# Kernel optimization log

Measured on AMD Instinct MI355X. Metric: run time of the kernel, lower is better.

The kernel has to match this reference:

```python
import jax, jax.numpy as jnp
import numpy as np


def _gcn(x, src, dst, W, b, M):
    # GCNConv: out = D^{-1/2} (A+I) D^{-1/2} X W + b, messages flow src->dst
    xw = x @ W  # [M, D]
    loops = jnp.arange(M)
    s = jnp.concatenate([src, loops])
    d = jnp.concatenate([dst, loops])
    deg = jax.ops.segment_sum(jnp.ones_like(s, x.dtype), d, num_segments=M)
    dinv = jnp.where(deg > 0, jax.lax.rsqrt(jnp.maximum(deg, 1.0)), 0.0)
    norm = dinv[s] * dinv[d]  # [Eg+M]
    return jax.ops.segment_sum(norm[:, None] * xw[s], d, num_segments=M) + b


def _graph_cross_attention(values, k, q, e_src, e_dst, N):
    # gather-dot, segment softmax over destination tokens, scatter-sum of values
    scale = jnp.sqrt(jnp.asarray(k.shape[1], k.dtype))
    dots = (q[e_dst] * k[e_src]).sum(-1) / scale  # [Ea]
    m = jax.ops.segment_max(dots, e_dst, num_segments=N)
    m = jnp.where(jnp.isfinite(m), m, 0.0)
    w = jnp.exp(dots - m[e_dst])
    den = jax.ops.segment_sum(w, e_dst, num_segments=N)
    w = w / jnp.where(den > 0, den, 1.0)[e_dst]
    return jax.ops.segment_sum(w[:, None] * values[e_src], e_dst, num_segments=N)


def reference(token_embeddings, tokens2edges, edge_index, e2t_src, e2t_dst,
              W_gnn, b_gnn, Wk, bk, Wq, bq, Wl, bl, gate_a, gate_b):
    N = token_embeddings.shape[1]
    M = tokens2edges.shape[1]

    def per_sample(t, t2e, ei, es, ed):
        edge_emb = t[t2e]                                  # [M, D] gather
        edge_emb = _gcn(edge_emb, ei[0], ei[1], W_gnn, b_gnn, M)
        k = edge_emb @ Wk + bk                             # [M, 64]
        q = t @ Wq + bq                                    # [N, 64]
        gatt = _graph_cross_attention(edge_emb, k, q, es, ed, N)  # [N, D]
        new = t + jnp.tanh(gate_a) * gatt
        new = new + jnp.tanh(gate_b) * (new @ Wl + bl)
        return new

    return jax.vmap(per_sample)(token_embeddings, tokens2edges, edge_index, e2t_src, e2t_dst)


def setup_inputs() -> dict:
    B, N, M, Eg, Ea, D, DK = 4, 4096, 16384, 65536, 65536, 512, 64
    key = jax.random.key(0)
    ks = jax.random.split(key, 16)
    s = 0.05  # weight scale to keep activations well-conditioned
    return {
        "token_embeddings": jax.random.normal(ks[0], (B, N, D), jnp.float32),
        "tokens2edges": jax.random.randint(ks[1], (B, M), 0, N),
        "edge_index": jax.random.randint(ks[2], (B, 2, Eg), 0, M),
        "e2t_src": jax.random.randint(ks[3], (B, Ea), 0, M),
        "e2t_dst": jax.random.randint(ks[4], (B, Ea), 0, N),
        "W_gnn": jax.random.normal(ks[5], (D, D), jnp.float32) * s,
        "b_gnn": jax.random.normal(ks[6], (D,), jnp.float32) * s,
        "Wk": jax.random.normal(ks[7], (D, DK), jnp.float32) * s,
        "bk": jax.random.normal(ks[8], (DK,), jnp.float32) * s,
        "Wq": jax.random.normal(ks[9], (D, DK), jnp.float32) * s,
        "bq": jax.random.normal(ks[10], (DK,), jnp.float32) * s,
        "Wl": jax.random.normal(ks[11], (D, D), jnp.float32) * s,
        "bl": jax.random.normal(ks[12], (D,), jnp.float32) * s,
        "gate_a": jax.random.normal(ks[13], (1,), jnp.float32),
        "gate_b": jax.random.normal(ks[14], (1,), jnp.float32),
    }
```

## Files before the change

### kernel.cpp

```cpp
#include <hip/hip_runtime.h>
#include <math.h>

#define BB 4
#define NT 4096
#define ME 16384
#define EG 65536
#define EA 65536
#define DD 512
#define DKK 64

using bf16x8 = __attribute__((ext_vector_type(8))) short;
using f32x4  = __attribute__((ext_vector_type(4))) float;

static __device__ __forceinline__ unsigned short f2bf(float f) {
    unsigned u = __float_as_uint(f);
    u += 0x7fffu + ((u >> 16) & 1u);
    return (unsigned short)(u >> 16);
}
static __device__ __forceinline__ float bf2f(unsigned short u) {
    return __uint_as_float((unsigned)u << 16);
}
static __device__ __forceinline__ void acc8(float* a, uint4 v, float s) {
    a[0] += s * __uint_as_float(v.x << 16);
    a[1] += s * __uint_as_float(v.x & 0xffff0000u);
    a[2] += s * __uint_as_float(v.y << 16);
    a[3] += s * __uint_as_float(v.y & 0xffff0000u);
    a[4] += s * __uint_as_float(v.z << 16);
    a[5] += s * __uint_as_float(v.z & 0xffff0000u);
    a[6] += s * __uint_as_float(v.w << 16);
    a[7] += s * __uint_as_float(v.w & 0xffff0000u);
}
static __device__ __forceinline__ uint4 pack8(const float* a) {
    uint4 o;
    o.x = (unsigned)f2bf(a[0]) | ((unsigned)f2bf(a[1]) << 16);
    o.y = (unsigned)f2bf(a[2]) | ((unsigned)f2bf(a[3]) << 16);
    o.z = (unsigned)f2bf(a[4]) | ((unsigned)f2bf(a[5]) << 16);
    o.w = (unsigned)f2bf(a[6]) | ((unsigned)f2bf(a[7]) << 16);
    return o;
}

__global__ void k_hist2(const int* __restrict__ ei_all, const int* __restrict__ ed_all,
                        int* __restrict__ cntG, int* __restrict__ cntA) {
    int i = blockIdx.x * 256 + threadIdx.x;
    if (i < BB * EG) {
        int b = i >> 16, e = i & (EG - 1);
        int dst = ei_all[(size_t)b * 2 * EG + EG + e];
        atomicAdd(&cntG[b * ME + dst], 1);
    } else {
        int j = i - BB * EG;
        atomicAdd(&cntA[(j >> 16) * NT + ed_all[j]], 1);
    }
}

__global__ __launch_bounds__(1024) void k_scan2(
    const int* __restrict__ cntG, int* __restrict__ offsG, int* __restrict__ curG,
    float* __restrict__ dinv,
    const int* __restrict__ cntA, int* __restrict__ offsA, int* __restrict__ curA) {
    __shared__ int sums[1024];
    int tid = threadIdx.x;
    int bid = blockIdx.x;
    const int* cnt;
    int *offs, *cur;
    float* dv = nullptr;
    int C, nk;
    if (bid < BB) {
        cnt = cntG + bid * ME; offs = offsG + bid * (ME + 1); cur = curG + bid * ME;
        dv = dinv + bid * ME; C = ME / 1024; nk = ME;
    } else {
        int b = bid - BB;
        cnt = cntA + b * NT; offs = offsA + b * (NT + 1); cur = curA + b * NT;
        C = NT / 1024; nk = NT;
    }
    int local[16];
    int tot = 0;
    for (int i = 0; i < C; ++i) { local[i] = cnt[tid * C + i]; tot += local[i]; }
    sums[tid] = tot;
    __syncthreads();
    for (int d = 1; d < 1024; d <<= 1) {
        int v = (tid >= d) ? sums[tid - d] : 0;
        __syncthreads();
        sums[tid] += v;
        __syncthreads();
    }
    int run = sums[tid] - tot;
    for (int i = 0; i < C; ++i) {
        int idx = tid * C + i;
        offs[idx] = run;
        cur[idx] = run;
        if (dv) dv[idx] = rsqrtf((float)local[i] + 1.0f);
        run += local[i];
    }
    if (tid == 1023) offs[nk] = run;
}

__global__ void k_fill2(const int* __restrict__ ei_all, const int* __restrict__ es_all,
                        const int* __restrict__ ed_all, const int* __restrict__ t2e_all,
                        const float* __restrict__ dinv,
                        int* __restrict__ curG, int2* __restrict__ csrG,
                        int* __restrict__ curA, int2* __restrict__ csrA) {
    int i = blockIdx.x * 256 + threadIdx.x;
    if (i < BB * EG) {
        int b = i >> 16, e = i & (EG - 1);
        const int* ei = ei_all + (size_t)b * 2 * EG;
        int s = ei[e], d = ei[EG + e];
        int p = atomicAdd(&curG[b * ME + d], 1);
        int2 v;
        v.x = t2e_all[(b << 14) + s];
        v.y = __float_as_int(dinv[b * ME + s]);
        csrG[(size_t)b * EG + p] = v;
    } else {
        int j = i - BB * EG;
        int b = j >> 16;
        int p = atomicAdd(&curA[b * NT + ed_all[j]], 1);
        int2 v;
        v.x = es_all[j];
        v.y = ed_all[j];
        csrA[(size_t)b * EA + p] = v;
    }
}

__global__ void k_cast(const float* __restrict__ x, unsigned short* __restrict__ xb) {
    long i = (long)blockIdx.x * blockDim.x + threadIdx.x;
    float4 v = *(const float4*)(x + (i << 2));
    ushort4 o;
    o.x = f2bf(v.x); o.y = f2bf(v.y); o.z = f2bf(v.z); o.w = f2bf(v.w);
    *(ushort4*)(xb + (i << 2)) = o;
}

__global__ void k_wt(const float* __restrict__ W, unsigned short* __restrict__ Wt) {
    int i = blockIdx.x * 256 + threadIdx.x;
    int n = i >> 9, k = i & 511;
    Wt[i] = f2bf(W[((long)k << 9) + n]);
}
__global__ void k_wtT(const float* __restrict__ Wgnn, const float* __restrict__ Wgk,
                      const float* __restrict__ Wq, unsigned short* __restrict__ BtT) {
    int i = blockIdx.x * 256 + threadIdx.x;
    int n = i >> 9, k = i & 511;
    float v;
    if (n < 512)      v = Wgnn[((long)k << 9) + n];
    else if (n < 576) v = Wgk[k * 64 + (n - 512)];
    else              v = Wq[k * 64 + (n - 576)];
    BtT[i] = f2bf(v);
}
__global__ void k_bias(const float* __restrict__ bgnn, const float* __restrict__ Wk,
                       const float* __restrict__ bk, const float* __restrict__ bq,
                       float* __restrict__ biasG, float* __restrict__ bias640) {
    int tid = threadIdx.x;
    if (tid < 512) { biasG[tid] = bgnn[tid]; bias640[tid] = 0.0f; return; }
    if (tid < 576) {
        int n = tid - 512;
        float s = bk[n];
        for (int k = 0; k < DD; ++k) s += bgnn[k] * Wk[k * 64 + n];
        biasG[tid] = s;
        bias640[tid] = 0.0f;
        return;
    }
    bias640[tid] = bq[tid - 576];
}

__global__ __launch_bounds__(256, 2) void gemm_token(
    const unsigned short* __restrict__ A, const unsigned short* __restrict__ BtT,
    const float* __restrict__ bias640, unsigned short* __restrict__ Xg,
    unsigned short* __restrict__ Xk, unsigned short* __restrict__ qmatb)
{
    __shared__ short As[64 * 32];
    __shared__ short Bs[320 * 32];
    int tid = threadIdx.x;
    int lane = tid & 63;
    int w = tid >> 6;
    long bm = (long)blockIdx.x * 64;
    int bcol = blockIdx.y * 320;
    const unsigned short* Bblk = BtT + (long)bcol * DD;

    f32x4 acc[4][5] = {};

    for (int k0 = 0; k0 < DD; k0 += 32) {
        {
            int s = tid;
            int r = s >> 2;
            int gc = ((s & 3) ^ ((s >> 3) & 3)) * 8;
            __builtin_amdgcn_global_load_lds(
                (const __attribute__((address_space(1))) unsigned int*)(A + (bm + r) * DD + k0 + gc),
                (__attribute__((address_space(3))) unsigned int*)(As + s * 8), 16, 0, 0);
        }
#pragma unroll
        for (int i = 0; i < 5; ++i) {
            int s = tid + i * 256;
            int r = s >> 2;
            int gc = ((s & 3) ^ ((s >> 3) & 3)) * 8;
            __builtin_amdgcn_global_load_lds(
                (const __attribute__((address_space(1))) unsigned int*)(Bblk + (long)r * DD + k0 + gc),
                (__attribute__((address_space(3))) unsigned int*)(Bs + s * 8), 16, 0, 0);
        }
        __syncthreads();

        int cq = lane >> 4;
        bf16x8 af[4];
#pragma unroll
        for (int rb = 0; rb < 4; ++rb) {
            int r = rb * 16 + (lane & 15);
            af[rb] = *(const bf16x8*)&As[(r * 4 + (cq ^ ((r >> 1) & 3))) * 8];
        }
#pragma unroll
        for (int cb = 0; cb < 5; ++cb) {
            int r = w * 80 + cb * 16 + (lane & 15);
            bf16x8 bf = *(const bf16x8*)&Bs[(r * 4 + (cq ^ ((r >> 1) & 3))) * 8];
#pragma unroll
            for (int rb = 0; rb < 4; ++rb)
                acc[rb][cb] = __builtin_amdgcn_mfma_f32_16x16x32_bf16(af[rb], bf, acc[rb][cb], 0, 0, 0);
        }
        __syncthreads();
    }

#pragma unroll
    for (int rb = 0; rb < 4; ++rb) {
        long row0 = bm + rb * 16 + ((lane >> 4) << 2);
#pragma unroll
        for (int cb = 0; cb < 5; ++cb) {
            int col = bcol + w * 80 + cb * 16 + (lane & 15);
            float bv = bias640[col];
            if (col < 512) {
#pragma unroll
                for (int r = 0; r < 4; ++r)
                    Xg[(row0 + r) * DD + col] = f2bf(acc[rb][cb][r] + bv);
            } else if (col < 576) {
#pragma unroll
                for (int r = 0; r < 4; ++r)
                    Xk[(row0 + r) * DKK + (col - 512)] = f2bf(acc[rb][cb][r] + bv);
            } else {
#pragma unroll
                for (int r = 0; r < 4; ++r)
                    qmatb[(row0 + r) * DKK + (col - 576)] = f2bf(acc[rb][cb][r] + bv);
            }
        }
    }
}

__global__ __launch_bounds__(256) void k_gcn_gather(
    const unsigned short* __restrict__ Xg, const unsigned short* __restrict__ Xk,
    const int* __restrict__ t2e_all, const float* __restrict__ dinv,
    const int* __restrict__ offsG, const int2* __restrict__ csrG,
    const float* __restrict__ biasG,
    unsigned short* __restrict__ eeb, unsigned short* __restrict__ kmatb)
{
    int mg = (blockIdx.x * 256 + threadIdx.x) >> 6;
    int lane = threadIdx.x & 63;
    int b = mg >> 14;
    int m = mg & (ME - 1);
    const int* offs = offsG + b * (ME + 1);
    const int2* csr = csrG + (size_t)b * EG;
    const unsigned short* gl = Xg + (((long)b * NT) << 9) + lane * 8;
    const unsigned short* kl = Xk + ((long)b * NT) * DKK + lane;

    float dm = dinv[mg];
    int self = t2e_all[mg];
    uint4 vself = *(const uint4*)(gl + ((long)self << 9));
    float kself = bf2f(kl[(long)self * DKK]);

    float a[8] = {0, 0, 0, 0, 0, 0, 0, 0};
    float ak = 0.0f;
    int p = offs[m], end = offs[m + 1];
    for (; p + 4 <= end; p += 4) {
        int2 e0 = csr[p], e1 = csr[p + 1], e2 = csr[p + 2], e3 = csr[p + 3];
        uint4 r0 = *(const uint4*)(gl + ((long)e0.x << 9));
        uint4 r1 = *(const uint4*)(gl + ((long)e1.x << 9));
        uint4 r2 = *(const uint4*)(gl + ((long)e2.x << 9));
        uint4 r3 = *(const uint4*)(gl + ((long)e3.x << 9));
        float k0 = bf2f(kl[(long)e0.x * DKK]);
        float k1 = bf2f(kl[(long)e1.x * DKK]);
        float k2 = bf2f(kl[(long)e2.x * DKK]);
        float k3 = bf2f(kl[(long)e3.x * DKK]);
        float w0 = __int_as_float(e0.y), w1 = __int_as_float(e1.y);
        float w2 = __int_as_float(e2.y), w3 = __int_as_float(e3.y);
        acc8(a, r0, w0); ak += w0 * k0;
        acc8(a, r1, w1); ak += w1 * k1;
        acc8(a, r2, w2); ak += w2 * k2;
        acc8(a, r3, w3); ak += w3 * k3;
    }
    for (; p < end; ++p) {
        int2 e = csr[p];
        float w = __int_as_float(e.y);
        acc8(a, *(const uint4*)(gl + ((long)e.x << 9)), w);
        ak += w * bf2f(kl[(long)e.x * DKK]);
    }
    acc8(a, vself, dm);
    ak += dm * kself;

    const float* bg = biasG + lane * 8;
    float4 b0 = *(const float4*)bg;
    float4 b1 = *(const float4*)(bg + 4);
    a[0] = dm * a[0] + b0.x; a[1] = dm * a[1] + b0.y;
    a[2] = dm * a[2] + b0.z; a[3] = dm * a[3] + b0.w;
    a[4] = dm * a[4] + b1.x; a[5] = dm * a[5] + b1.y;
    a[6] = dm * a[6] + b1.z; a[7] = dm * a[7] + b1.w;
    *(uint4*)(eeb + ((long)mg << 9) + lane * 8) = pack8(a);
    kmatb[(long)mg * DKK + lane] = f2bf(dm * ak + biasG[512 + lane]);
}

__global__ void k_dots(const unsigned short* __restrict__ kmatb,
                       const unsigned short* __restrict__ qmatb,
                       const int2* __restrict__ csrA, float* __restrict__ wbuf) {
    int p = blockIdx.x * 256 + threadIdx.x;
    int b = p >> 16;
    int2 sd = csrA[p];
    const uint4* kr = (const uint4*)(kmatb + ((long)(b * ME + sd.x) << 6));
    const uint4* qr = (const uint4*)(qmatb + ((long)(b * NT + sd.y) << 6));
    float dot = 0.0f;
#pragma unroll
    for (int j = 0; j < 8; ++j) {
        uint4 kv = kr[j];
        uint4 qv = qr[j];
        dot += __uint_as_float(kv.x << 16) * __uint_as_float(qv.x << 16)
             + __uint_as_float(kv.x & 0xffff0000u) * __uint_as_float(qv.x & 0xffff0000u)
             + __uint_as_float(kv.y << 16) * __uint_as_float(qv.y << 16)
             + __uint_as_float(kv.y & 0xffff0000u) * __uint_as_float(qv.y & 0xffff0000u)
             + __uint_as_float(kv.z << 16) * __uint_as_float(qv.z << 16)
             + __uint_as_float(kv.z & 0xffff0000u) * __uint_as_float(qv.z & 0xffff0000u)
             + __uint_as_float(kv.w << 16) * __uint_as_float(qv.w << 16)
             + __uint_as_float(kv.w & 0xffff0000u) * __uint_as_float(qv.w & 0xffff0000u);
    }
    wbuf[p] = expf(dot * 0.125f);
}

__global__ __launch_bounds__(256) void k_att_gather(
    const unsigned short* __restrict__ eeb, const float* __restrict__ wbuf,
    const int* __restrict__ offsA, const int2* __restrict__ csrA,
    const float* __restrict__ t_all, const float* __restrict__ ga,
    float* __restrict__ out, unsigned short* __restrict__ nb)
{
    int ng = (blockIdx.x * 256 + threadIdx.x) >> 6;
    int lane = threadIdx.x & 63;
    int b = ng >> 12;
    int n = ng & (NT - 1);
    const int* offs = offsA + b * (NT + 1);
    const int2* csr = csrA + (size_t)b * EA;
    const float* wb = wbuf + (size_t)b * EA;
    const unsigned short* el = eeb + (((size_t)b * ME) << 9) + lane * 8;

    float a[8] = {0, 0, 0, 0, 0, 0, 0, 0};
    float den = 0.0f;
    int p = offs[n], end = offs[n + 1];
    for (; p + 4 <= end; p += 4) {
        int s0 = csr[p].x, s1 = csr[p + 1].x, s2 = csr[p + 2].x, s3 = csr[p + 3].x;
        float w0 = wb[p], w1 = wb[p + 1], w2 = wb[p + 2], w3 = wb[p + 3];
        uint4 r0 = *(const uint4*)(el + ((long)s0 << 9));
        uint4 r1 = *(const uint4*)(el + ((long)s1 << 9));
        uint4 r2 = *(const uint4*)(el + ((long)s2 << 9));
        uint4 r3 = *(const uint4*)(el + ((long)s3 << 9));
        den += w0 + w1 + w2 + w3;
        acc8(a, r0, w0);
        acc8(a, r1, w1);
        acc8(a, r2, w2);
        acc8(a, r3, w3);
    }
    for (; p < end; ++p) {
        int s = csr[p].x;
        float w = wb[p];
        den += w;
        acc8(a, *(const uint4*)(el + ((long)s << 9)), w);
    }
    float g = tanhf(ga[0]);
    float inv = den > 0.0f ? g / den : 0.0f;
    const float* tr = t_all + ((long)ng << 9) + lane * 8;
    float4 t0 = *(const float4*)tr;
    float4 t1 = *(const float4*)(tr + 4);
    float o[8];
    o[0] = t0.x + inv * a[0]; o[1] = t0.y + inv * a[1];
    o[2] = t0.z + inv * a[2]; o[3] = t0.w + inv * a[3];
    o[4] = t1.x + inv * a[4]; o[5] = t1.y + inv * a[5];
    o[6] = t1.z + inv * a[6]; o[7] = t1.w + inv * a[7];
    float* op = out + ((long)ng << 9) + lane * 8;
    *(float4*)op = make_float4(o[0], o[1], o[2], o[3]);
    *(float4*)(op + 4) = make_float4(o[4], o[5], o[6], o[7]);
    *(uint4*)(nb + ((long)ng << 9) + lane * 8) = pack8(o);
}

__global__ __launch_bounds__(256, 2) void gemm_final(
    const unsigned short* __restrict__ A, const unsigned short* __restrict__ Bt,
    const float* __restrict__ bias, float* __restrict__ Cf, const float* __restrict__ gs)
{
    constexpr int CB = 8;
    constexpr int BROWS = 2 * CB * 16;
    __shared__ short As[128 * 32];
    __shared__ short Bs[BROWS * 32];
    int tid = threadIdx.x;
    int lane = tid & 63;
    int w = tid >> 6;
    int wm = w >> 1, wn = w & 1;
    long bm = (long)blockIdx.x * 128;
    int bcol = blockIdx.y * BROWS;
    const unsigned short* Bblk = Bt + (long)bcol * DD;

    f32x4 acc[4][CB] = {};

    for (int k0 = 0; k0 < DD; k0 += 32) {
#pragma unroll
        for (int i = 0; i < 2; ++i) {
            int s = tid + i * 256;
            int r = s >> 2;
            int gc = ((s & 3) ^ ((s >> 3) & 3)) * 8;
            __builtin_amdgcn_global_load_lds(
                (const __attribute__((address_space(1))) unsigned int*)(A + (bm + r) * DD + k0 + gc),
                (__attribute__((address_space(3))) unsigned int*)(As + s * 8), 16, 0, 0);
        }
#pragma unroll
        for (int i = 0; i < CB / 2; ++i) {
            int s = tid + i * 256;
            int r = s >> 2;
            int gc = ((s & 3) ^ ((s >> 3) & 3)) * 8;
            __builtin_amdgcn_global_load_lds(
                (const __attribute__((address_space(1))) unsigned int*)(Bblk + (long)r * DD + k0 + gc),
                (__attribute__((address_space(3))) unsigned int*)(Bs + s * 8), 16, 0, 0);
        }
        __syncthreads();

        int cq = lane >> 4;
        bf16x8 af[4];
#pragma unroll
        for (int rb = 0; rb < 4; ++rb) {
            int r = wm * 64 + rb * 16 + (lane & 15);
            af[rb] = *(const bf16x8*)&As[(r * 4 + (cq ^ ((r >> 1) & 3))) * 8];
        }
#pragma unroll
        for (int cb = 0; cb < CB; ++cb) {
            int r = wn * (CB * 16) + cb * 16 + (lane & 15);
            bf16x8 bf = *(const bf16x8*)&Bs[(r * 4 + (cq ^ ((r >> 1) & 3))) * 8];
#pragma unroll
            for (int rb = 0; rb < 4; ++rb)
                acc[rb][cb] = __builtin_amdgcn_mfma_f32_16x16x32_bf16(af[rb], bf, acc[rb][cb], 0, 0, 0);
        }
        __syncthreads();
    }

    float g = tanhf(gs[0]);
#pragma unroll
    for (int rb = 0; rb < 4; ++rb) {
        long row0 = bm + wm * 64 + rb * 16 + ((lane >> 4) << 2);
#pragma unroll
        for (int cb = 0; cb < CB; ++cb) {
            int col = bcol + wn * (CB * 16) + cb * 16 + (lane & 15);
            float bv = bias[col];
#pragma unroll
            for (int r = 0; r < 4; ++r)
                Cf[(row0 + r) * DD + col] += g * (acc[rb][cb][r] + bv);
        }
    }
}

__global__ void gemm_tiled(const float* __restrict__ A, const float* __restrict__ Bw,
                           float* __restrict__ C, int K, int Nc) {
    __shared__ float As[16][64];
    __shared__ float Bs[16][64];
    int tid = threadIdx.x;
    int tx = tid & 15, ty = tid >> 4;
    int bm = blockIdx.x * 64, bn = blockIdx.y * 64;
    float acc[4][4] = {};
    int arow = bm + (tid >> 2);
    long aoff = (long)arow * K;
    int kk0 = (tid & 3) * 4;
    int arowl = tid >> 2;
    for (int k0 = 0; k0 < K; k0 += 16) {
        float4 av = *(const float4*)(A + aoff + k0 + kk0);
        As[kk0 + 0][arowl] = av.x;
        As[kk0 + 1][arowl] = av.y;
        As[kk0 + 2][arowl] = av.z;
        As[kk0 + 3][arowl] = av.w;
        float4 bv = *(const float4*)(Bw + (long)(k0 + (tid >> 4)) * Nc + bn + (tid & 15) * 4);
        *(float4*)&Bs[tid >> 4][(tid & 15) * 4] = bv;
        __syncthreads();
#pragma unroll
        for (int k = 0; k < 16; ++k) {
            float4 a = *(const float4*)&As[k][ty * 4];
            float4 b = *(const float4*)&Bs[k][tx * 4];
            acc[0][0] += a.x * b.x; acc[0][1] += a.x * b.y; acc[0][2] += a.x * b.z; acc[0][3] += a.x * b.w;
            acc[1][0] += a.y * b.x; acc[1][1] += a.y * b.y; acc[1][2] += a.y * b.z; acc[1][3] += a.y * b.w;
            acc[2][0] += a.z * b.x; acc[2][1] += a.z * b.y; acc[2][2] += a.z * b.z; acc[2][3] += a.z * b.w;
            acc[3][0] += a.w * b.x; acc[3][1] += a.w * b.y; acc[3][2] += a.w * b.z; acc[3][3] += a.w * b.w;
        }
        __syncthreads();
    }
#pragma unroll
    for (int i = 0; i < 4; ++i)
        *(float4*)(C + (long)(bm + ty * 4 + i) * Nc + bn + tx * 4) =
            make_float4(acc[i][0], acc[i][1], acc[i][2], acc[i][3]);
}

extern "C" void kernel_launch(void* const* d_in, const int* in_sizes, int n_in,
                              void* d_out, int out_size, void* d_ws, size_t ws_size,
                              hipStream_t stream) {
    const float* t_all   = (const float*)d_in[0];
    const int*   t2e_all = (const int*)d_in[1];
    const int*   ei_all  = (const int*)d_in[2];
    const int*   es_all  = (const int*)d_in[3];
    const int*   ed_all  = (const int*)d_in[4];
    const float* Wgnn    = (const float*)d_in[5];
    const float* bgnn    = (const float*)d_in[6];
    const float* Wk      = (const float*)d_in[7];
    const float* bk      = (const float*)d_in[8];
    const float* Wq      = (const float*)d_in[9];
    const float* bq      = (const float*)d_in[10];
    const float* Wl      = (const float*)d_in[11];
    const float* bl      = (const float*)d_in[12];
    const float* ga      = (const float*)d_in[13];
    const float* gb      = (const float*)d_in[14];
    float* out = (float*)d_out;

    char* wsb = (char*)d_ws;
    size_t off = 0;
    unsigned short* eeb   = (unsigned short*)(wsb + off); off += (size_t)BB * ME * DD * 2;
    unsigned short* tb    = (unsigned short*)(wsb + off); off += (size_t)BB * NT * DD * 2;
    unsigned short* Xg    = (unsigned short*)(wsb + off); off += (size_t)BB * NT * DD * 2;
    unsigned short* nb    = (unsigned short*)(wsb + off); off += (size_t)BB * NT * DD * 2;
    unsigned short* Xk    = (unsigned short*)(wsb + off); off += (size_t)BB * NT * DKK * 2;
    unsigned short* qmatb = (unsigned short*)(wsb + off); off += (size_t)BB * NT * DKK * 2;
    unsigned short* kmatb = (unsigned short*)(wsb + off); off += (size_t)BB * ME * DKK * 2;
    unsigned short* BtT   = (unsigned short*)(wsb + off); off += (size_t)640 * DD * 2;
    unsigned short* Wlt   = (unsigned short*)(wsb + off); off += (size_t)DD * DD * 2;
    float* Wgk     = (float*)(wsb + off); off += (size_t)DD * DKK * 4;
    float* biasG   = (float*)(wsb + off); off += 576 * 4;
    float* bias640 = (float*)(wsb + off); off += 640 * 4;
    float* dinv  = (float*)(wsb + off); off += (size_t)BB * ME * 4;
    float* wbuf  = (float*)(wsb + off); off += (size_t)BB * EA * 4;
    int* cntG  = (int*)(wsb + off); off += (size_t)BB * ME * 4;
    int* cntA  = (int*)(wsb + off); off += (size_t)BB * NT * 4;
    int* offsG = (int*)(wsb + off); off += (size_t)BB * (ME + 1) * 4;
    int* curG  = (int*)(wsb + off); off += (size_t)BB * ME * 4;
    int2* csrG = (int2*)(wsb + off); off += (size_t)BB * EG * 8;
    int* offsA = (int*)(wsb + off); off += (size_t)BB * (NT + 1) * 4;
    int* curA  = (int*)(wsb + off); off += (size_t)BB * NT * 4;
    int2* csrA = (int2*)(wsb + off); off += (size_t)BB * EA * 8;

    gemm_tiled<<<dim3(DD / 64, 1), 256, 0, stream>>>(Wgnn, Wk, Wgk, DD, DKK);
    k_wt<<<(DD * DD) / 256, 256, 0, stream>>>(Wl, Wlt);
    k_wtT<<<(640 * DD) / 256, 256, 0, stream>>>(Wgnn, Wgk, Wq, BtT);
    k_bias<<<1, 640, 0, stream>>>(bgnn, Wk, bk, bq, biasG, bias640);

    hipMemsetAsync(cntG, 0, (size_t)BB * (ME + NT) * 4, stream);
    k_hist2<<<(BB * (EG + EA)) / 256, 256, 0, stream>>>(ei_all, ed_all, cntG, cntA);
    k_scan2<<<2 * BB, 1024, 0, stream>>>(cntG, offsG, curG, dinv, cntA, offsA, curA);
    k_fill2<<<(BB * (EG + EA)) / 256, 256, 0, stream>>>(
        ei_all, es_all, ed_all, t2e_all, dinv, curG, csrG, curA, csrA);

    k_cast<<<(int)(((long)BB * NT * DD / 4) / 256), 256, 0, stream>>>(t_all, tb);
    gemm_token<<<dim3((BB * NT) / 64, 2), 256, 0, stream>>>(tb, BtT, bias640, Xg, Xk, qmatb);

    k_gcn_gather<<<(BB * ME * 64) / 256, 256, 0, stream>>>(
        Xg, Xk, t2e_all, dinv, offsG, csrG, biasG, eeb, kmatb);

    k_dots<<<(BB * EA) / 256, 256, 0, stream>>>(kmatb, qmatb, csrA, wbuf);
    k_att_gather<<<(BB * NT * 64) / 256, 256, 0, stream>>>(
        eeb, wbuf, offsA, csrA, t_all, ga, out, nb);

    gemm_final<<<dim3((BB * NT) / 128, 2), 256, 0, stream>>>(nb, Wlt, bl, out, gb);
}
```

Baseline: 387.7 us.

## Split gather kernels across two waves per row with deeper unrolled loads

The GCN and attention gather kernels now assign two wavefronts per output row, each handling half of the 512 feature columns with 8-byte loads. The edge loops are unrolled to 8 or 16 independent loads using clamped indices and zeroed weights, which puts more memory requests in flight. k_dots now writes the source index together with the exp weight into one packed int2 buffer, so the attention gather reads a single stream instead of csrA plus wbuf. The two weight-transpose kernels are merged into one launch. The trade-off is twice as many waves, duplicated index reads per row, and wasted work on padded tail iterations.

```diff
diff --git a/kernel.cpp b/kernel.cpp
--- a/kernel.cpp
+++ b/kernel.cpp
@@ -20,22 +20,16 @@
 static __device__ __forceinline__ float bf2f(unsigned short u) {
     return __uint_as_float((unsigned)u << 16);
 }
-static __device__ __forceinline__ void acc8(float* a, uint4 v, float s) {
+static __device__ __forceinline__ void acc4(float* a, uint2 v, float s) {
     a[0] += s * __uint_as_float(v.x << 16);
     a[1] += s * __uint_as_float(v.x & 0xffff0000u);
     a[2] += s * __uint_as_float(v.y << 16);
     a[3] += s * __uint_as_float(v.y & 0xffff0000u);
-    a[4] += s * __uint_as_float(v.z << 16);
-    a[5] += s * __uint_as_float(v.z & 0xffff0000u);
-    a[6] += s * __uint_as_float(v.w << 16);
-    a[7] += s * __uint_as_float(v.w & 0xffff0000u);
-}
-static __device__ __forceinline__ uint4 pack8(const float* a) {
-    uint4 o;
+}
+static __device__ __forceinline__ uint2 pack4(const float* a) {
+    uint2 o;
     o.x = (unsigned)f2bf(a[0]) | ((unsigned)f2bf(a[1]) << 16);
     o.y = (unsigned)f2bf(a[2]) | ((unsigned)f2bf(a[3]) << 16);
-    o.z = (unsigned)f2bf(a[4]) | ((unsigned)f2bf(a[5]) << 16);
-    o.w = (unsigned)f2bf(a[6]) | ((unsigned)f2bf(a[7]) << 16);
     return o;
 }
 
@@ -127,20 +121,22 @@
     *(ushort4*)(xb + (i << 2)) = o;
 }
 
-__global__ void k_wt(const float* __restrict__ W, unsigned short* __restrict__ Wt) {
+__global__ void k_wtT(const float* __restrict__ Wgnn, const float* __restrict__ Wgk,
+                      const float* __restrict__ Wq, const float* __restrict__ Wl,
+                      unsigned short* __restrict__ BtT, unsigned short* __restrict__ Wlt) {
     int i = blockIdx.x * 256 + threadIdx.x;
-    int n = i >> 9, k = i & 511;
-    Wt[i] = f2bf(W[((long)k << 9) + n]);
-}
-__global__ void k_wtT(const float* __restrict__ Wgnn, const float* __restrict__ Wgk,
-                      const float* __restrict__ Wq, unsigned short* __restrict__ BtT) {
-    int i = blockIdx.x * 256 + threadIdx.x;
-    int n = i >> 9, k = i & 511;
-    float v;
-    if (n < 512)      v = Wgnn[((long)k << 9) + n];
-    else if (n < 576) v = Wgk[k * 64 + (n - 512)];
-    else              v = Wq[k * 64 + (n - 576)];
-    BtT[i] = f2bf(v);
+    if (i < 640 * 512) {
+        int n = i >> 9, k = i & 511;
+        float v;
+        if (n < 512)      v = Wgnn[((long)k << 9) + n];
+        else if (n < 576) v = Wgk[k * 64 + (n - 512)];
+        else              v = Wq[k * 64 + (n - 576)];
+        BtT[i] = f2bf(v);
+    } else {
+        int j = i - 640 * 512;
+        int n = j >> 9, k = j & 511;
+        Wlt[j] = f2bf(Wl[((long)k << 9) + n]);
+    }
 }
 __global__ void k_bias(const float* __restrict__ bgnn, const float* __restrict__ Wk,
                        const float* __restrict__ bk, const float* __restrict__ bq,
@@ -243,63 +239,61 @@
     const float* __restrict__ biasG,
     unsigned short* __restrict__ eeb, unsigned short* __restrict__ kmatb)
 {
-    int mg = (blockIdx.x * 256 + threadIdx.x) >> 6;
+    int wid = (blockIdx.x * 256 + threadIdx.x) >> 6;
     int lane = threadIdx.x & 63;
+    int h = wid & 1;
+    int mg = wid >> 1;
     int b = mg >> 14;
     int m = mg & (ME - 1);
     const int* offs = offsG + b * (ME + 1);
     const int2* csr = csrG + (size_t)b * EG;
-    const unsigned short* gl = Xg + (((long)b * NT) << 9) + lane * 8;
+    const unsigned short* gl = Xg + (((long)b * NT) << 9) + (h << 8) + lane * 4;
     const unsigned short* kl = Xk + ((long)b * NT) * DKK + lane;
 
     float dm = dinv[mg];
     int self = t2e_all[mg];
-    uint4 vself = *(const uint4*)(gl + ((long)self << 9));
-    float kself = bf2f(kl[(long)self * DKK]);
-
-    float a[8] = {0, 0, 0, 0, 0, 0, 0, 0};
+    uint2 vself = *(const uint2*)(gl + ((long)self << 9));
+    float kself = (h == 0) ? bf2f(kl[(long)self * DKK]) : 0.0f;
+
+    float a[4] = {0, 0, 0, 0};
     float ak = 0.0f;
-    int p = offs[m], end = offs[m + 1];
-    for (; p + 4 <= end; p += 4) {
-        int2 e0 = csr[p], e1 = csr[p + 1], e2 = csr[p + 2], e3 = csr[p + 3];
-        uint4 r0 = *(const uint4*)(gl + ((long)e0.x << 9));
-        uint4 r1 = *(const uint4*)(gl + ((long)e1.x << 9));
-        uint4 r2 = *(const uint4*)(gl + ((long)e2.x << 9));
-        uint4 r3 = *(const uint4*)(gl + ((long)e3.x << 9));
-        float k0 = bf2f(kl[(long)e0.x * DKK]);
-        float k1 = bf2f(kl[(long)e1.x * DKK]);
-        float k2 = bf2f(kl[(long)e2.x * DKK]);
-        float k3 = bf2f(kl[(long)e3.x * DKK]);
-        float w0 = __int_as_float(e0.y), w1 = __int_as_float(e1.y);
-        float w2 = __int_as_float(e2.y), w3 = __int_as_float(e3.y);
-        acc8(a, r0, w0); ak += w0 * k0;
-        acc8(a, r1, w1); ak += w1 * k1;
-        acc8(a, r2, w2); ak += w2 * k2;
-        acc8(a, r3, w3); ak += w3 * k3;
-    }
-    for (; p < end; ++p) {
-        int2 e = csr[p];
-        float w = __int_as_float(e.y);
-        acc8(a, *(const uint4*)(gl + ((long)e.x << 9)), w);
-        ak += w * bf2f(kl[(long)e.x * DKK]);
-    }
-    acc8(a, vself, dm);
-    ak += dm * kself;
-
-    const float* bg = biasG + lane * 8;
+    int p0 = offs[m], end = offs[m + 1];
+    int e1m = end - 1;
+    for (int p = p0; p < end; p += 8) {
+        int2 e[8];
+#pragma unroll
+        for (int i = 0; i < 8; ++i) e[i] = csr[min(p + i, e1m)];
+        uint2 r[8];
+#pragma unroll
+        for (int i = 0; i < 8; ++i) r[i] = *(const uint2*)(gl + ((long)e[i].x << 9));
+        float kv[8];
+        if (h == 0) {
+#pragma unroll
+            for (int i = 0; i < 8; ++i) kv[i] = bf2f(kl[(long)e[i].x * DKK]);
+        }
+#pragma unroll
+        for (int i = 0; i < 8; ++i) {
+            float w = (p + i < end) ? __int_as_float(e[i].y) : 0.0f;
+            acc4(a, r[i], w);
+            if (h == 0) ak += w * kv[i];
+        }
+    }
+    acc4(a, vself, dm);
+
+    const float* bg = biasG + (h << 8) + lane * 4;
     float4 b0 = *(const float4*)bg;
-    float4 b1 = *(const float4*)(bg + 4);
     a[0] = dm * a[0] + b0.x; a[1] = dm * a[1] + b0.y;
     a[2] = dm * a[2] + b0.z; a[3] = dm * a[3] + b0.w;
-    a[4] = dm * a[4] + b1.x; a[5] = dm * a[5] + b1.y;
-    a[6] = dm * a[6] + b1.z; a[7] = dm * a[7] + b1.w;
-    *(uint4*)(eeb + ((long)mg << 9) + lane * 8) = pack8(a);
-    kmatb[(long)mg * DKK + lane] = f2bf(dm * ak + biasG[512 + lane]);
+    *(uint2*)(eeb + ((long)mg << 9) + (h << 8) + lane * 4) = pack4(a);
+    if (h == 0) {
+        ak += dm * kself;
+        kmatb[(long)mg * DKK + lane] = f2bf(dm * ak + biasG[512 + lane]);
+    }
 }
 
 __global__ void k_dots(const unsigned short* __restrict__ kmatb,
                        const unsigned short* __restrict__ qmatb,
-                       const int2* __restrict__ csrA, float* __restrict__ wbuf) {
+                       const int2* __restrict__ csrA, int2* __restrict__ swbuf) {
     int p = blockIdx.x * 256 + threadIdx.x;
     int b = p >> 16;
     int2 sd = csrA[p];
@@ -319,60 +313,56 @@
              + __uint_as_float(kv.w << 16) * __uint_as_float(qv.w << 16)
              + __uint_as_float(kv.w & 0xffff0000u) * __uint_as_float(qv.w & 0xffff0000u);
     }
-    wbuf[p] = expf(dot * 0.125f);
+    int2 o;
+    o.x = sd.x;
+    o.y = __float_as_int(expf(dot * 0.125f));
+    swbuf[p] = o;
 }
 
 __global__ __launch_bounds__(256) void k_att_gather(
-    const unsigned short* __restrict__ eeb, const float* __restrict__ wbuf,
-    const int* __restrict__ offsA, const int2* __restrict__ csrA,
+    const unsigned short* __restrict__ eeb, const int2* __restrict__ swbuf,
+    const int* __restrict__ offsA,
     const float* __restrict__ t_all, const float* __restrict__ ga,
     float* __restrict__ out, unsigned short* __restrict__ nb)
 {
-    int ng = (blockIdx.x * 256 + threadIdx.x) >> 6;
+    int wid = (blockIdx.x * 256 + threadIdx.x) >> 6;
     int lane = threadIdx.x & 63;
+    int h = wid & 1;
+    int ng = wid >> 1;
     int b = ng >> 12;
     int n = ng & (NT - 1);
     const int* offs = offsA + b * (NT + 1);
-    const int2* csr = csrA + (size_t)b * EA;
-    const float* wb = wbuf + (size_t)b * EA;
-    const unsigned short* el = eeb + (((size_t)b * ME) << 9) + lane * 8;
-
-    float a[8] = {0, 0, 0, 0, 0, 0, 0, 0};
+    const int2* swb = swbuf + (size_t)b * EA;
+    const unsigned short* el = eeb + (((size_t)b * ME) << 9) + (h << 8) + lane * 4;
+
+    float a[4] = {0, 0, 0, 0};
     float den = 0.0f;
-    int p = offs[n], end = offs[n + 1];
-    for (; p + 4 <= end; p += 4) {
-        int s0 = csr[p].x, s1 = csr[p + 1].x, s2 = csr[p + 2].x, s3 = csr[p + 3].x;
-        float w0 = wb[p], w1 = wb[p + 1], w2 = wb[p + 2], w3 = wb[p + 3];
-        uint4 r0 = *(const uint4*)(el + ((long)s0 << 9));
-        uint4 r1 = *(const uint4*)(el + ((long)s1 << 9));
-        uint4 r2 = *(const uint4*)(el + ((long)s2 << 9));
-        uint4 r3 = *(const uint4*)(el + ((long)s3 << 9));
-        den += w0 + w1 + w2 + w3;
-        acc8(a, r0, w0);
-        acc8(a, r1, w1);
-        acc8(a, r2, w2);
-        acc8(a, r3, w3);
-    }
-    for (; p < end; ++p) {
-        int s = csr[p].x;
-        float w = wb[p];
-        den += w;
-        acc8(a, *(const uint4*)(el + ((long)s << 9)), w);
+    int p0 = offs[n], end = offs[n + 1];
+    int e1m = end - 1;
+    for (int p = p0; p < end; p += 16) {
+        int2 e[16];
+#pragma unroll
+        for (int i = 0; i < 16; ++i) e[i] = swb[min(p + i, e1m)];
+        uint2 r[16];
+#pragma unroll
+        for (int i = 0; i < 16; ++i) r[i] = *(const uint2*)(el + ((long)e[i].x << 9));
+#pragma unroll
+        for (int i = 0; i < 16; ++i) {
+            float w = (p + i < end) ? __int_as_float(e[i].y) : 0.0f;
+            den += w;
+            acc4(a, r[i], w);
+        }
     }
     float g = tanhf(ga[0]);
     float inv = den > 0.0f ? g / den : 0.0f;
-    const float* tr = t_all + ((long)ng << 9) + lane * 8;
+    const float* tr = t_all + ((long)ng << 9) + (h << 8) + lane * 4;
     float4 t0 = *(const float4*)tr;
-    float4 t1 = *(const float4*)(tr + 4);
-    float o[8];
+    float o[4];
     o[0] = t0.x + inv * a[0]; o[1] = t0.y + inv * a[1];
     o[2] = t0.z + inv * a[2]; o[3] = t0.w + inv * a[3];
-    o[4] = t1.x + inv * a[4]; o[5] = t1.y + inv * a[5];
-    o[6] = t1.z + inv * a[6]; o[7] = t1.w + inv * a[7];
-    float* op = out + ((long)ng << 9) + lane * 8;
+    float* op = out + ((long)ng << 9) + (h << 8) + lane * 4;
     *(float4*)op = make_float4(o[0], o[1], o[2], o[3]);
-    *(float4*)(op + 4) = make_float4(o[4], o[5], o[6], o[7]);
-    *(uint4*)(nb + ((long)ng << 9) + lane * 8) = pack8(o);
+    *(uint2*)(nb + ((long)ng << 9) + (h << 8) + lane * 4) = pack4(o);
 }
 
 __global__ __launch_bounds__(256, 2) void gemm_final(
@@ -520,7 +510,7 @@
     float* biasG   = (float*)(wsb + off); off += 576 * 4;
     float* bias640 = (float*)(wsb + off); off += 640 * 4;
     float* dinv  = (float*)(wsb + off); off += (size_t)BB * ME * 4;
-    float* wbuf  = (float*)(wsb + off); off += (size_t)BB * EA * 4;
+    int2* swbuf  = (int2*)(wsb + off); off += (size_t)BB * EA * 8;
     int* cntG  = (int*)(wsb + off); off += (size_t)BB * ME * 4;
     int* cntA  = (int*)(wsb + off); off += (size_t)BB * NT * 4;
     int* offsG = (int*)(wsb + off); off += (size_t)BB * (ME + 1) * 4;
@@ -531,8 +521,7 @@
     int2* csrA = (int2*)(wsb + off); off += (size_t)BB * EA * 8;
 
     gemm_tiled<<<dim3(DD / 64, 1), 256, 0, stream>>>(Wgnn, Wk, Wgk, DD, DKK);
-    k_wt<<<(DD * DD) / 256, 256, 0, stream>>>(Wl, Wlt);
-    k_wtT<<<(640 * DD) / 256, 256, 0, stream>>>(Wgnn, Wgk, Wq, BtT);
+    k_wtT<<<(1152 * DD) / 256, 256, 0, stream>>>(Wgnn, Wgk, Wq, Wl, BtT, Wlt);
     k_bias<<<1, 640, 0, stream>>>(bgnn, Wk, bk, bq, biasG, bias640);
 
     hipMemsetAsync(cntG, 0, (size_t)BB * (ME + NT) * 4, stream);
@@ -544,12 +533,12 @@
     k_cast<<<(int)(((long)BB * NT * DD / 4) / 256), 256, 0, stream>>>(t_all, tb);
     gemm_token<<<dim3((BB * NT) / 64, 2), 256, 0, stream>>>(tb, BtT, bias640, Xg, Xk, qmatb);
 
-    k_gcn_gather<<<(BB * ME * 64) / 256, 256, 0, stream>>>(
+    k_gcn_gather<<<(BB * ME * 2 * 64) / 256, 256, 0, stream>>>(
         Xg, Xk, t2e_all, dinv, offsG, csrG, biasG, eeb, kmatb);
 
-    k_dots<<<(BB * EA) / 256, 256, 0, stream>>>(kmatb, qmatb, csrA, wbuf);
-    k_att_gather<<<(BB * NT * 64) / 256, 256, 0, stream>>>(
-        eeb, wbuf, offsA, csrA, t_all, ga, out, nb);
+    k_dots<<<(BB * EA) / 256, 256, 0, stream>>>(kmatb, qmatb, csrA, swbuf);
+    k_att_gather<<<(BB * NT * 2 * 64) / 256, 256, 0, stream>>>(
+        eeb, swbuf, offsA, t_all, ga, out, nb);
 
     gemm_final<<<dim3((BB * NT) / 128, 2), 256, 0, stream>>>(nb, Wlt, bl, out, gb);
 }
```

New measurement: 460.7 us. 18.9% more time.
